# Kernel tuning notes

Hardware: AMD Instinct MI355X
Metric: run time of the kernel (lower is better)

Reference implementation:

```python
import jax, jax.numpy as jnp
import numpy as np

IN_F = 128
OUT_F = 128
ALPHA = 0.2  # LeakyReLU negative slope


def _xavier_uniform(key, shape, gain):
    fan_in, fan_out = shape[0], shape[1]
    bound = gain * np.sqrt(6.0 / (fan_in + fan_out))
    return jax.random.uniform(key, shape, jnp.float32, -bound, bound)


def setup_inputs() -> dict:
    key = jax.random.key(0)
    kx, kw, ka = jax.random.split(key, 3)
    x = jax.random.normal(kx, (8, 2048, IN_F), jnp.float32)
    W = _xavier_uniform(kw, (IN_F, OUT_F), 1.414)
    a = _xavier_uniform(ka, (2 * OUT_F, 1), 1.414)
    return {"x": x, "W": W, "a": a}


def reference(x, W, a):
    B, T, _ = x.shape
    h = jnp.matmul(x, W)  # [B, T, F]
    # e_ij = leakyrelu([h_i ; h_j] @ a) = leakyrelu(h_i @ a1 + h_j @ a2)
    a1 = a[:OUT_F, 0]   # [F]
    a2 = a[OUT_F:, 0]   # [F]
    f1 = h @ a1         # [B, T]
    f2 = h @ a2         # [B, T]
    e = f1[:, :, None] + f2[:, None, :]          # [B, T, T]
    e = jnp.where(e >= 0, e, ALPHA * e)          # LeakyReLU
    attention = jax.nn.softmax(e, axis=-1)       # [B, T, T]
    # dropout is identity at inference
    return jnp.matmul(attention, h)              # [B, T, F]
```

## Files before the change

kernel.cpp:

```cpp
#include <hip/hip_runtime.h>
#include <hip/hip_bf16.h>

typedef __attribute__((ext_vector_type(8))) short short8;
typedef __attribute__((ext_vector_type(8))) unsigned short ushort8;
typedef __attribute__((ext_vector_type(16))) float f32x16;

#define LOG2E 1.4426950408889634f
#define MFMA32(a, b, c) __builtin_amdgcn_mfma_f32_32x32x16_bf16((a), (b), (c), 0, 0, 0)
#define ZERO16 {0.f,0.f,0.f,0.f,0.f,0.f,0.f,0.f,0.f,0.f,0.f,0.f,0.f,0.f,0.f,0.f}

__device__ __forceinline__ unsigned short bfbits(float f) {
    __hip_bfloat16 h = __float2bfloat16(f);
    return __builtin_bit_cast(unsigned short, h);
}
__device__ __forceinline__ float bf2f(unsigned short u) {
    unsigned v = ((unsigned)u) << 16;
    return __builtin_bit_cast(float, v);
}

__global__ __launch_bounds__(256) void gat_wt(const float* __restrict__ W,
                                              unsigned short* __restrict__ WT2h,
                                              unsigned short* __restrict__ WT2l) {
    const int k16 = blockIdx.x;
    const int d = threadIdx.x >> 1;
    const int klo8 = (threadIdx.x & 1) * 8;
    ushort8 vh, vl;
#pragma unroll
    for (int q = 0; q < 8; ++q) {
        float f = W[(k16 * 16 + klo8 + q) * 128 + d];
        unsigned short hb = bfbits(f);
        vh[q] = hb;
        vl[q] = bfbits(f - bf2f(hb));
    }
    size_t base = (size_t)k16 * 2048 + d * 16 + klo8;
    *(ushort8*)(WT2h + base) = vh;
    *(ushort8*)(WT2l + base) = vl;
}

__global__ __launch_bounds__(256) void gat_h(const float* __restrict__ x,
                                             const unsigned short* __restrict__ WT2h,
                                             const unsigned short* __restrict__ WT2l,
                                             const float* __restrict__ a,
                                             unsigned short* __restrict__ HT2h,
                                             float* __restrict__ f1l,
                                             float* __restrict__ f2l) {
    __shared__ unsigned short xs_h[32][132];
    __shared__ unsigned short xs_l[32][132];
    __shared__ float hs[32][130];
    __shared__ float red[2][32][8];
    const int tid = threadIdx.x;
    const int lane = tid & 63;
    const int wv = tid >> 6;
    const int l31 = lane & 31;
    const int hi = lane >> 5;
    const int t0 = blockIdx.x * 32;
    const int c0 = wv * 32;

#pragma unroll
    for (int r8 = 0; r8 < 4; ++r8) {
        int row = r8 * 8 + (tid >> 5);
        int c4 = (tid & 31) * 4;
        float4 v = *(const float4*)(x + (size_t)(t0 + row) * 128 + c4);
        float f[4] = {v.x, v.y, v.z, v.w};
#pragma unroll
        for (int q = 0; q < 4; ++q) {
            unsigned short hb = bfbits(f[q]);
            xs_h[row][c4 + q] = hb;
            xs_l[row][c4 + q] = bfbits(f[q] - bf2f(hb));
        }
    }
    __syncthreads();

    f32x16 p0 = ZERO16, p1 = ZERO16, p2 = ZERO16;
    const unsigned short* bph = WT2h + (c0 + l31) * 16 + 8 * hi;
    const unsigned short* bpl = WT2l + (c0 + l31) * 16 + 8 * hi;
#pragma unroll
    for (int kk8 = 0; kk8 < 8; ++kk8) {
        short8 ah = *(const short8*)&xs_h[l31][kk8 * 16 + 8 * hi];
        short8 al = *(const short8*)&xs_l[l31][kk8 * 16 + 8 * hi];
        short8 bh = __builtin_bit_cast(short8, *(const ushort8*)(bph + kk8 * 2048));
        short8 bl = __builtin_bit_cast(short8, *(const ushort8*)(bpl + kk8 * 2048));
        p0 = MFMA32(ah, bh, p0);
        p1 = MFMA32(al, bh, p1);
        p2 = MFMA32(ah, bl, p2);
    }
#pragma unroll
    for (int r = 0; r < 16; ++r) {
        int crow = (r & 3) + 8 * (r >> 2) + 4 * hi;
        hs[crow][c0 + l31] = p0[r] + p1[r] + p2[r];
    }
    __syncthreads();
    {
        const int d = tid & 127, half = tid >> 7;
        ushort8 h0, h1;
#pragma unroll
        for (int j = 0; j < 8; ++j) h0[j] = bfbits(hs[half * 16 + j][d]);
#pragma unroll
        for (int j = 0; j < 8; ++j) h1[j] = bfbits(hs[half * 16 + 8 + j][d]);
        const int b = t0 >> 11;
        const int tloc = t0 & 2047;
        size_t base = (size_t)b * 262144 + (size_t)(tloc / 16 + half) * 2048 + d * 16;
        *(ushort8*)(HT2h + base) = h0;
        *(ushort8*)(HT2h + base + 8) = h1;
    }
    {
        const int r = tid & 31, seg = tid >> 5;
        float s1 = 0.f, s2 = 0.f;
#pragma unroll
        for (int i = 0; i < 16; ++i) {
            float hv = hs[r][seg * 16 + i];
            s1 += hv * a[seg * 16 + i];
            s2 += hv * a[128 + seg * 16 + i];
        }
        red[0][r][seg] = s1;
        red[1][r][seg] = s2;
    }
    __syncthreads();
    if (tid < 32) {
        float s1 = 0.f, s2 = 0.f;
#pragma unroll
        for (int g = 0; g < 8; ++g) { s1 += red[0][tid][g]; s2 += red[1][tid][g]; }
        f1l[t0 + tid] = s1 * LOG2E;
        f2l[t0 + tid] = s2 * LOG2E;
    }
}

__global__ __launch_bounds__(256) void gat_f2max(const float* __restrict__ f2l,
                                                 float* __restrict__ f2m) {
    const int b = blockIdx.x;
    const int tid = threadIdx.x;
    float m = -3.4e38f;
    for (int j = tid; j < 2048; j += 256) m = fmaxf(m, f2l[b * 2048 + j]);
#pragma unroll
    for (int o = 1; o < 64; o <<= 1) m = fmaxf(m, __shfl_xor(m, o, 64));
    __shared__ float wm_[4];
    if ((tid & 63) == 0) wm_[tid >> 6] = m;
    __syncthreads();
    if (tid == 0) f2m[b] = fmaxf(fmaxf(wm_[0], wm_[1]), fmaxf(wm_[2], wm_[3]));
}

__global__ __launch_bounds__(512) void gat_attn(const unsigned short* __restrict__ HT2h,
                                                const float* __restrict__ f1l,
                                                const float* __restrict__ f2l,
                                                const float* __restrict__ f2m,
                                                float* __restrict__ out) {
    __shared__ float lred[3][2][64][64];
    __shared__ float sps[4][64];
    const int bid = blockIdx.x;
    const int b = bid & 7;
    const int tile = bid >> 3;
    const int tid = threadIdx.x;
    const int lane = tid & 63;
    const int wv = tid >> 6;
    const int wj = wv >> 1;
    const int wn = wv & 1;
    const int l31 = lane & 31;
    const int hi = lane >> 5;
    const int koff = hi * 8;

    const float fm = f2m[b];
    const float f1m0 = f1l[b * 2048 + tile * 64 + l31];
    const float f1m1 = f1l[b * 2048 + tile * 64 + 32 + l31];
    const float tm0 = f1m0 + fm, tm1 = f1m1 + fm;
    const float ml0 = fmaxf(tm0, 0.2f * tm0);
    const float ml1 = fmaxf(tm1, 0.2f * tm1);
    const float A0 = f1m0 - ml0, B0 = 0.2f * f1m0 - ml0;
    const float A1 = f1m1 - ml1, B1 = 0.2f * f1m1 - ml1;

    const int jbase = wj * 512;
    const float* f2b = f2l + b * 2048 + jbase;
    const int c0 = wn * 64;
    const unsigned short* ph = HT2h + (size_t)b * 262144
                             + (size_t)(jbase / 16) * 2048 + (c0 + l31) * 16 + koff;

    f32x16 a00 = ZERO16, a01 = ZERO16, a10 = ZERO16, a11 = ZERO16;
    float sp0 = 0.f, sp1 = 0.f;

    float4 fva = *(const float4*)(f2b + koff);
    float4 fvb = *(const float4*)(f2b + koff + 4);
    uint4 vh0 = *(const uint4*)(ph);
    uint4 vh1 = *(const uint4*)(ph + 512);

    for (int jl = 0; jl < 512; jl += 16) {
        const int jn = (jl + 16) & 511;
        float4 nfa = *(const float4*)(f2b + jn + koff);
        float4 nfb = *(const float4*)(f2b + jn + koff + 4);
        uint4 nh0 = *(const uint4*)(ph + (size_t)jn * 128);
        uint4 nh1 = *(const uint4*)(ph + (size_t)jn * 128 + 512);

        float fv[8] = {fva.x, fva.y, fva.z, fva.w, fvb.x, fvb.y, fvb.z, fvb.w};
        short8 af0, af1;
#pragma unroll
        for (int q = 0; q < 8; ++q) {
            float g = 0.2f * fv[q];
            float p0 = __builtin_amdgcn_exp2f(fmaxf(A0 + fv[q], B0 + g));
            float p1 = __builtin_amdgcn_exp2f(fmaxf(A1 + fv[q], B1 + g));
            sp0 += p0; sp1 += p1;
            af0[q] = (short)bfbits(p0);
            af1[q] = (short)bfbits(p1);
        }
        a00 = MFMA32(af0, __builtin_bit_cast(short8, vh0), a00);
        a01 = MFMA32(af0, __builtin_bit_cast(short8, vh1), a01);
        a10 = MFMA32(af1, __builtin_bit_cast(short8, vh0), a10);
        a11 = MFMA32(af1, __builtin_bit_cast(short8, vh1), a11);

        fva = nfa; fvb = nfb;
        vh0 = nh0; vh1 = nh1;
    }

    sp0 += __shfl_xor(sp0, 32, 64);
    sp1 += __shfl_xor(sp1, 32, 64);
    if (wn == 0 && lane < 32) { sps[wj][l31] = sp0; sps[wj][32 + l31] = sp1; }

    if (wj > 0) {
#pragma unroll
        for (int r = 0; r < 16; ++r) {
            int crow = (r & 3) + 8 * (r >> 2) + 4 * hi;
            lred[wj - 1][wn][crow][l31] = a00[r];
            lred[wj - 1][wn][crow][32 + l31] = a01[r];
            lred[wj - 1][wn][32 + crow][l31] = a10[r];
            lred[wj - 1][wn][32 + crow][32 + l31] = a11[r];
        }
    }
    __syncthreads();

    if (wj == 0) {
        const size_t obase = ((size_t)b * 2048 + (size_t)tile * 64) * 128 + c0 + l31;
#pragma unroll
        for (int r = 0; r < 16; ++r) {
            int crow = (r & 3) + 8 * (r >> 2) + 4 * hi;
            float s00 = a00[r] + lred[0][wn][crow][l31]
                      + lred[1][wn][crow][l31] + lred[2][wn][crow][l31];
            float s01 = a01[r] + lred[0][wn][crow][32 + l31]
                      + lred[1][wn][crow][32 + l31] + lred[2][wn][crow][32 + l31];
            float s10 = a10[r] + lred[0][wn][32 + crow][l31]
                      + lred[1][wn][32 + crow][l31] + lred[2][wn][32 + crow][l31];
            float s11 = a11[r] + lred[0][wn][32 + crow][32 + l31]
                      + lred[1][wn][32 + crow][32 + l31] + lred[2][wn][32 + crow][32 + l31];
            float inv0 = 1.0f / (sps[0][crow] + sps[1][crow] + sps[2][crow] + sps[3][crow]);
            float inv1 = 1.0f / (sps[0][32 + crow] + sps[1][32 + crow]
                               + sps[2][32 + crow] + sps[3][32 + crow]);
            out[obase + (size_t)crow * 128] = s00 * inv0;
            out[obase + (size_t)crow * 128 + 32] = s01 * inv0;
            out[obase + (size_t)(32 + crow) * 128] = s10 * inv1;
            out[obase + (size_t)(32 + crow) * 128 + 32] = s11 * inv1;
        }
    }
}

extern "C" void kernel_launch(void* const* d_in, const int* in_sizes, int n_in,
                              void* d_out, int out_size, void* d_ws, size_t ws_size,
                              hipStream_t stream) {
    const float* x = (const float*)d_in[0];
    const float* W = (const float*)d_in[1];
    const float* a = (const float*)d_in[2];
    float* out = (float*)d_out;

    unsigned short* WT2h = (unsigned short*)d_ws;
    unsigned short* WT2l = WT2h + 128 * 128;
    unsigned short* HT2h = WT2l + 128 * 128;
    float* f1l = (float*)(HT2h + (size_t)8 * 128 * 2048);
    float* f2l = f1l + 16384;
    float* f2m = f2l + 16384;

    gat_wt<<<8, 256, 0, stream>>>(W, WT2h, WT2l);
    gat_h<<<512, 256, 0, stream>>>(x, WT2h, WT2l, a, HT2h, f1l, f2l);
    gat_f2max<<<8, 256, 0, stream>>>(f2l, f2m);
    gat_attn<<<256, 512, 0, stream>>>(HT2h, f1l, f2l, f2m, out);
}
```

Baseline: 42.42 us.

## Fuse f2 max into projection via atomicMax and repartition attention waves over keys

Drops the separate f2max kernel: the projection kernel reduces each 32-row block's f2 maximum with shuffles and publishes it through an order-preserving unsigned atomicMax. gat_wt zeroes the keys first. The attention kernel now splits the key dimension across all 8 waves, each owning the full 128-column output with 8 accumulators, instead of 4 key-slices by 2 column halves. A tree reduction through shared memory combines the partial sums. This saves one launch and halves the per-wave A-operand exp work, at the cost of doubled accumulator registers, a larger LDS buffer, and several extra barriers in the reduction.

```diff
diff --git a/kernel.cpp b/kernel.cpp
--- a/kernel.cpp
+++ b/kernel.cpp
@@ -20,7 +20,9 @@
 
 __global__ __launch_bounds__(256) void gat_wt(const float* __restrict__ W,
                                               unsigned short* __restrict__ WT2h,
-                                              unsigned short* __restrict__ WT2l) {
+                                              unsigned short* __restrict__ WT2l,
+                                              unsigned int* __restrict__ f2mk) {
+    if (blockIdx.x == 0 && threadIdx.x < 8) f2mk[threadIdx.x] = 0u;
     const int k16 = blockIdx.x;
     const int d = threadIdx.x >> 1;
     const int klo8 = (threadIdx.x & 1) * 8;
@@ -43,7 +45,8 @@
                                              const float* __restrict__ a,
                                              unsigned short* __restrict__ HT2h,
                                              float* __restrict__ f1l,
-                                             float* __restrict__ f2l) {
+                                             float* __restrict__ f2l,
+                                             unsigned int* __restrict__ f2mk) {
     __shared__ unsigned short xs_h[32][132];
     __shared__ unsigned short xs_l[32][132];
     __shared__ float hs[32][130];
@@ -121,72 +124,72 @@
 #pragma unroll
         for (int g = 0; g < 8; ++g) { s1 += red[0][tid][g]; s2 += red[1][tid][g]; }
         f1l[t0 + tid] = s1 * LOG2E;
-        f2l[t0 + tid] = s2 * LOG2E;
-    }
-}
-
-__global__ __launch_bounds__(256) void gat_f2max(const float* __restrict__ f2l,
-                                                 float* __restrict__ f2m) {
-    const int b = blockIdx.x;
-    const int tid = threadIdx.x;
-    float m = -3.4e38f;
-    for (int j = tid; j < 2048; j += 256) m = fmaxf(m, f2l[b * 2048 + j]);
-#pragma unroll
-    for (int o = 1; o < 64; o <<= 1) m = fmaxf(m, __shfl_xor(m, o, 64));
-    __shared__ float wm_[4];
-    if ((tid & 63) == 0) wm_[tid >> 6] = m;
-    __syncthreads();
-    if (tid == 0) f2m[b] = fmaxf(fmaxf(wm_[0], wm_[1]), fmaxf(wm_[2], wm_[3]));
-}
-
-__global__ __launch_bounds__(512) void gat_attn(const unsigned short* __restrict__ HT2h,
-                                                const float* __restrict__ f1l,
-                                                const float* __restrict__ f2l,
-                                                const float* __restrict__ f2m,
-                                                float* __restrict__ out) {
-    __shared__ float lred[3][2][64][64];
-    __shared__ float sps[4][64];
+        float f2v = s2 * LOG2E;
+        f2l[t0 + tid] = f2v;
+        float m = f2v;
+#pragma unroll
+        for (int o = 1; o < 32; o <<= 1) m = fmaxf(m, __shfl_xor(m, o, 32));
+        if (tid == 0) {
+            unsigned int bits = __builtin_bit_cast(unsigned int, m);
+            unsigned int key = (bits & 0x80000000u) ? ~bits : (bits | 0x80000000u);
+            atomicMax(f2mk + (t0 >> 11), key);
+        }
+    }
+}
+
+__global__ __launch_bounds__(512, 2) void gat_attn(const unsigned short* __restrict__ HT2h,
+                                                   const float* __restrict__ f1l,
+                                                   const float* __restrict__ f2l,
+                                                   const unsigned int* __restrict__ f2mk,
+                                                   float* __restrict__ out) {
+    __shared__ float lred[4][64][132];
+    __shared__ float sps[8][64];
+    __shared__ float sinv[64];
     const int bid = blockIdx.x;
     const int b = bid & 7;
     const int tile = bid >> 3;
     const int tid = threadIdx.x;
     const int lane = tid & 63;
     const int wv = tid >> 6;
-    const int wj = wv >> 1;
-    const int wn = wv & 1;
     const int l31 = lane & 31;
     const int hi = lane >> 5;
     const int koff = hi * 8;
 
-    const float fm = f2m[b];
-    const float f1m0 = f1l[b * 2048 + tile * 64 + l31];
-    const float f1m1 = f1l[b * 2048 + tile * 64 + 32 + l31];
+    const unsigned int kk = f2mk[b];
+    const unsigned int mbits = (kk & 0x80000000u) ? (kk & 0x7fffffffu) : ~kk;
+    const float fm = __builtin_bit_cast(float, mbits);
+
+    const int rowg = b * 2048 + tile * 64 + l31;
+    const float f1m0 = f1l[rowg];
+    const float f1m1 = f1l[rowg + 32];
     const float tm0 = f1m0 + fm, tm1 = f1m1 + fm;
     const float ml0 = fmaxf(tm0, 0.2f * tm0);
     const float ml1 = fmaxf(tm1, 0.2f * tm1);
     const float A0 = f1m0 - ml0, B0 = 0.2f * f1m0 - ml0;
     const float A1 = f1m1 - ml1, B1 = 0.2f * f1m1 - ml1;
 
-    const int jbase = wj * 512;
+    const int jbase = wv * 256;
     const float* f2b = f2l + b * 2048 + jbase;
-    const int c0 = wn * 64;
     const unsigned short* ph = HT2h + (size_t)b * 262144
-                             + (size_t)(jbase / 16) * 2048 + (c0 + l31) * 16 + koff;
-
-    f32x16 a00 = ZERO16, a01 = ZERO16, a10 = ZERO16, a11 = ZERO16;
+                             + (size_t)(jbase >> 4) * 2048 + l31 * 16 + koff;
+
+    f32x16 acc[2][4] = {{ZERO16, ZERO16, ZERO16, ZERO16},
+                        {ZERO16, ZERO16, ZERO16, ZERO16}};
     float sp0 = 0.f, sp1 = 0.f;
 
-    float4 fva = *(const float4*)(f2b + koff);
-    float4 fvb = *(const float4*)(f2b + koff + 4);
     uint4 vh0 = *(const uint4*)(ph);
     uint4 vh1 = *(const uint4*)(ph + 512);
-
-    for (int jl = 0; jl < 512; jl += 16) {
-        const int jn = (jl + 16) & 511;
-        float4 nfa = *(const float4*)(f2b + jn + koff);
-        float4 nfb = *(const float4*)(f2b + jn + koff + 4);
-        uint4 nh0 = *(const uint4*)(ph + (size_t)jn * 128);
-        uint4 nh1 = *(const uint4*)(ph + (size_t)jn * 128 + 512);
+    uint4 vh2 = *(const uint4*)(ph + 1024);
+    uint4 vh3 = *(const uint4*)(ph + 1536);
+
+    for (int it = 0; it < 16; ++it) {
+        const unsigned short* pn = ph + (size_t)((it + 1) & 15) * 2048;
+        uint4 nh0 = *(const uint4*)(pn);
+        uint4 nh1 = *(const uint4*)(pn + 512);
+        uint4 nh2 = *(const uint4*)(pn + 1024);
+        uint4 nh3 = *(const uint4*)(pn + 1536);
+        float4 fva = *(const float4*)(f2b + it * 16 + koff);
+        float4 fvb = *(const float4*)(f2b + it * 16 + koff + 4);
 
         float fv[8] = {fva.x, fva.y, fva.z, fva.w, fvb.x, fvb.y, fvb.z, fvb.w};
         short8 af0, af1;
@@ -199,51 +202,102 @@
             af0[q] = (short)bfbits(p0);
             af1[q] = (short)bfbits(p1);
         }
-        a00 = MFMA32(af0, __builtin_bit_cast(short8, vh0), a00);
-        a01 = MFMA32(af0, __builtin_bit_cast(short8, vh1), a01);
-        a10 = MFMA32(af1, __builtin_bit_cast(short8, vh0), a10);
-        a11 = MFMA32(af1, __builtin_bit_cast(short8, vh1), a11);
-
-        fva = nfa; fvb = nfb;
-        vh0 = nh0; vh1 = nh1;
+        acc[0][0] = MFMA32(af0, __builtin_bit_cast(short8, vh0), acc[0][0]);
+        acc[0][1] = MFMA32(af0, __builtin_bit_cast(short8, vh1), acc[0][1]);
+        acc[0][2] = MFMA32(af0, __builtin_bit_cast(short8, vh2), acc[0][2]);
+        acc[0][3] = MFMA32(af0, __builtin_bit_cast(short8, vh3), acc[0][3]);
+        acc[1][0] = MFMA32(af1, __builtin_bit_cast(short8, vh0), acc[1][0]);
+        acc[1][1] = MFMA32(af1, __builtin_bit_cast(short8, vh1), acc[1][1]);
+        acc[1][2] = MFMA32(af1, __builtin_bit_cast(short8, vh2), acc[1][2]);
+        acc[1][3] = MFMA32(af1, __builtin_bit_cast(short8, vh3), acc[1][3]);
+
+        vh0 = nh0; vh1 = nh1; vh2 = nh2; vh3 = nh3;
     }
 
     sp0 += __shfl_xor(sp0, 32, 64);
     sp1 += __shfl_xor(sp1, 32, 64);
-    if (wn == 0 && lane < 32) { sps[wj][l31] = sp0; sps[wj][32 + l31] = sp1; }
-
-    if (wj > 0) {
-#pragma unroll
-        for (int r = 0; r < 16; ++r) {
-            int crow = (r & 3) + 8 * (r >> 2) + 4 * hi;
-            lred[wj - 1][wn][crow][l31] = a00[r];
-            lred[wj - 1][wn][crow][32 + l31] = a01[r];
-            lred[wj - 1][wn][32 + crow][l31] = a10[r];
-            lred[wj - 1][wn][32 + crow][32 + l31] = a11[r];
-        }
-    }
-    __syncthreads();
-
-    if (wj == 0) {
-        const size_t obase = ((size_t)b * 2048 + (size_t)tile * 64) * 128 + c0 + l31;
-#pragma unroll
-        for (int r = 0; r < 16; ++r) {
-            int crow = (r & 3) + 8 * (r >> 2) + 4 * hi;
-            float s00 = a00[r] + lred[0][wn][crow][l31]
-                      + lred[1][wn][crow][l31] + lred[2][wn][crow][l31];
-            float s01 = a01[r] + lred[0][wn][crow][32 + l31]
-                      + lred[1][wn][crow][32 + l31] + lred[2][wn][crow][32 + l31];
-            float s10 = a10[r] + lred[0][wn][32 + crow][l31]
-                      + lred[1][wn][32 + crow][l31] + lred[2][wn][32 + crow][l31];
-            float s11 = a11[r] + lred[0][wn][32 + crow][32 + l31]
-                      + lred[1][wn][32 + crow][32 + l31] + lred[2][wn][32 + crow][32 + l31];
-            float inv0 = 1.0f / (sps[0][crow] + sps[1][crow] + sps[2][crow] + sps[3][crow]);
-            float inv1 = 1.0f / (sps[0][32 + crow] + sps[1][32 + crow]
-                               + sps[2][32 + crow] + sps[3][32 + crow]);
-            out[obase + (size_t)crow * 128] = s00 * inv0;
-            out[obase + (size_t)crow * 128 + 32] = s01 * inv0;
-            out[obase + (size_t)(32 + crow) * 128] = s10 * inv1;
-            out[obase + (size_t)(32 + crow) * 128 + 32] = s11 * inv1;
+    if (lane < 32) { sps[wv][l31] = sp0; sps[wv][32 + l31] = sp1; }
+
+    if (wv >= 4) {
+#pragma unroll
+        for (int r = 0; r < 16; ++r) {
+            int crow = (r & 3) + 8 * (r >> 2) + 4 * hi;
+#pragma unroll
+            for (int s = 0; s < 2; ++s)
+#pragma unroll
+                for (int c = 0; c < 4; ++c)
+                    lred[wv - 4][s * 32 + crow][c * 32 + l31] = acc[s][c][r];
+        }
+    }
+    __syncthreads();
+    if (wv < 4) {
+#pragma unroll
+        for (int r = 0; r < 16; ++r) {
+            int crow = (r & 3) + 8 * (r >> 2) + 4 * hi;
+#pragma unroll
+            for (int s = 0; s < 2; ++s)
+#pragma unroll
+                for (int c = 0; c < 4; ++c)
+                    acc[s][c][r] += lred[wv][s * 32 + crow][c * 32 + l31];
+        }
+    } else if (wv == 4) {
+        float tot = 0.f;
+#pragma unroll
+        for (int w = 0; w < 8; ++w) tot += sps[w][lane];
+        sinv[lane] = 1.0f / tot;
+    }
+    __syncthreads();
+    if (wv == 2 || wv == 3) {
+#pragma unroll
+        for (int r = 0; r < 16; ++r) {
+            int crow = (r & 3) + 8 * (r >> 2) + 4 * hi;
+#pragma unroll
+            for (int s = 0; s < 2; ++s)
+#pragma unroll
+                for (int c = 0; c < 4; ++c)
+                    lred[wv - 2][s * 32 + crow][c * 32 + l31] = acc[s][c][r];
+        }
+    }
+    __syncthreads();
+    if (wv < 2) {
+#pragma unroll
+        for (int r = 0; r < 16; ++r) {
+            int crow = (r & 3) + 8 * (r >> 2) + 4 * hi;
+#pragma unroll
+            for (int s = 0; s < 2; ++s)
+#pragma unroll
+                for (int c = 0; c < 4; ++c)
+                    acc[s][c][r] += lred[wv][s * 32 + crow][c * 32 + l31];
+        }
+    }
+    __syncthreads();
+    if (wv == 1) {
+#pragma unroll
+        for (int r = 0; r < 16; ++r) {
+            int crow = (r & 3) + 8 * (r >> 2) + 4 * hi;
+#pragma unroll
+            for (int s = 0; s < 2; ++s)
+#pragma unroll
+                for (int c = 0; c < 4; ++c)
+                    lred[0][s * 32 + crow][c * 32 + l31] = acc[s][c][r];
+        }
+    }
+    __syncthreads();
+    if (wv == 0) {
+        const size_t obase = ((size_t)b * 2048 + (size_t)tile * 64) * 128;
+#pragma unroll
+        for (int r = 0; r < 16; ++r) {
+            int crow = (r & 3) + 8 * (r >> 2) + 4 * hi;
+#pragma unroll
+            for (int s = 0; s < 2; ++s) {
+                int row = s * 32 + crow;
+                float iv = sinv[row];
+#pragma unroll
+                for (int c = 0; c < 4; ++c) {
+                    float v = acc[s][c][r] + lred[0][row][c * 32 + l31];
+                    out[obase + (size_t)row * 128 + c * 32 + l31] = v * iv;
+                }
+            }
         }
     }
 }
@@ -261,10 +315,9 @@
     unsigned short* HT2h = WT2l + 128 * 128;
     float* f1l = (float*)(HT2h + (size_t)8 * 128 * 2048);
     float* f2l = f1l + 16384;
-    float* f2m = f2l + 16384;
-
-    gat_wt<<<8, 256, 0, stream>>>(W, WT2h, WT2l);
-    gat_h<<<512, 256, 0, stream>>>(x, WT2h, WT2l, a, HT2h, f1l, f2l);
-    gat_f2max<<<8, 256, 0, stream>>>(f2l, f2m);
-    gat_attn<<<256, 512, 0, stream>>>(HT2h, f1l, f2l, f2m, out);
-}
+    unsigned int* f2mk = (unsigned int*)(f2l + 16384);
+
+    gat_wt<<<8, 256, 0, stream>>>(W, WT2h, WT2l, f2mk);
+    gat_h<<<512, 256, 0, stream>>>(x, WT2h, WT2l, a, HT2h, f1l, f2l, f2mk);
+    gat_attn<<<256, 512, 0, stream>>>(HT2h, f1l, f2l, f2mk, out);
+}
```

New measurement: 40.16 us. 1.06x faster.
